# Performance work log

Hardware: AMD Instinct MI355X
Metric: run time of the kernel (lower is better)

Reference implementation:

```python
import jax, jax.numpy as jnp
import numpy as np

K = 64      # neighbor_num (subgraph size)
TOPK = 10   # topk for sparse adjacency scatter
DN = 10     # density_neighbor


def _build_graphs(indexes, features):
    # compute_knn: inner-product top-K neighbor table over all N samples
    N, D = features.shape
    sim = features @ features.T                      # [N, N]
    _, ori0 = jax.lax.top_k(sim, K)                  # [N, K] neighbor indices
    # density: all_sim[n] = sum_{i<DN} <f_n, f_{ori0[n,i]}> / (4*DN)
    g = features[ori0[:, :DN]]                       # [N, DN, D]
    all_sim = jnp.einsum('nd,nkd->n', features, g) / (4.0 * DN)
    exp_sim = jnp.exp(all_sim)                       # [N]

    rows = jnp.arange(K)[:, None]                    # [K,1]

    def build_one(idx):
        nbr = ori0[idx]                              # [K] neighbors of query idx
        feat = features[nbr]                         # [K, D]
        neigh = ori0[nbr][:, :TOPK]                  # [K, TOPK]
        A = (feat @ features.T) * exp_sim[None, :]   # [K, N] density-reweighted sims
        # scatter only the topk entries of each row into sparse tmp
        tmp = jnp.zeros((K, N), features.dtype).at[rows, neigh].set(A[rows, neigh])
        adj = tmp @ (tmp.T > 0).astype(features.dtype)   # [K, K]
        adj = jax.nn.softmax(adj, axis=1)
        x = feat - feat[0]                           # center on query node
        return x, adj

    return jax.vmap(build_one)(indexes)              # [B,K,D], [B,K,K]


def _gconv(x, adj, W, b):
    # GraphConv with MeanAggregator: out = relu(concat([x, adj@x]) @ W + b)
    agg = jnp.einsum('bij,bjd->bid', adj, x)
    cat = jnp.concatenate([x, agg], axis=-1)
    return jax.nn.relu(jnp.einsum('bkd,df->bkf', cat, W) + b)


def setup_inputs() -> dict:
    key = jax.random.key(0)
    ks = jax.random.split(key, 16)
    N, D, NHID = 8192, 2048, 1024
    feats = jax.random.normal(ks[0], (N, D), dtype=jnp.float32)
    feats = feats / jnp.linalg.norm(feats, axis=1, keepdims=True)  # L2-normalized embeddings
    p = lambda k, shape: jax.random.normal(k, shape, dtype=jnp.float32) * 0.02
    return {
        'indexes': jax.random.randint(ks[1], (64,), 0, N, dtype=jnp.int64) if jax.config.jax_enable_x64 else jax.random.randint(ks[1], (64,), 0, N, dtype=jnp.int32),
        'features': feats,
        'labels': jax.random.randint(ks[2], (N,), 0, 1000, dtype=jnp.int32),
        'domain': 1,
        'W1': p(ks[3], (2 * D, NHID)), 'b1': jnp.zeros((NHID,), jnp.float32),
        'W2': p(ks[4], (2 * NHID, 512)), 'b2': jnp.zeros((512,), jnp.float32),
        'W3': p(ks[5], (2 * 512, 256)), 'b3': jnp.zeros((256,), jnp.float32),
        'W4': p(ks[6], (2 * 256, 256)), 'b4': jnp.zeros((256,), jnp.float32),
        'Wc1': p(ks[7], (256, 256)), 'bc1': jnp.zeros((256,), jnp.float32),
        'prelu_a': jnp.full((256,), 0.25, jnp.float32),
        'Wc2': p(ks[8], (256, 2)), 'bc2': jnp.zeros((2,), jnp.float32),
    }


def reference(indexes, features, labels, domain, W1, b1, W2, b2, W3, b3, W4, b4,
              Wc1, bc1, prelu_a, Wc2, bc2):
    # labels only used for the (optional) loss branch; domain=1 path implemented.
    xs, adjs = _build_graphs(indexes, features)      # built under no_grad in torch
    h = _gconv(xs, adjs, W1, b1)
    h = _gconv(h, adjs, W2, b2)
    h = _gconv(h, adjs, W3, b3)
    h = _gconv(h, adjs, W4, b4)
    h = h @ Wc1 + bc1
    h = jnp.where(h > 0, h, prelu_a * h)             # PReLU(256)
    pred = h @ Wc2 + bc2                             # [B, K, 2]
    return pred
```

## Files before the change

### kernel.cpp

```cpp
#include <hip/hip_runtime.h>
#include <hip/hip_bf16.h>
#include <math.h>

#define NROWS 8192
#define DFEAT 2048
#define KSEL  64
#define CHK   2048

typedef unsigned long long u64;
typedef __attribute__((ext_vector_type(8))) short bf16x8;
typedef __attribute__((ext_vector_type(4))) float f32x4;

__device__ __forceinline__ u64 umax64(u64 a, u64 b) { return a > b ? a : b; }

__device__ __forceinline__ void split2(float v, ushort& h, ushort& l) {
  __hip_bfloat16 bh = __float2bfloat16(v);
  float r = v - __bfloat162float(bh);
  __hip_bfloat16 bl = __float2bfloat16(r);
  h = *(ushort*)&bh; l = *(ushort*)&bl;
}

__device__ __forceinline__ u64 mkkey_vi(float v, int i) {
  unsigned u = __float_as_uint(v);
  u = ((int)u < 0) ? ~u : (u | 0x80000000u);
  return ((u64)u << 32) | (u64)(0xFFFFFFFFu - (unsigned)i);
}

__global__ __launch_bounds__(256) void k_split(const float* __restrict__ F, ushort* __restrict__ H,
                                               ushort* __restrict__ M, ushort* __restrict__ L) {
  const size_t i0 = ((size_t)blockIdx.x * 256 + threadIdx.x) * 4;
  float4 x = *(const float4*)(F + i0);
  float xs[4] = {x.x, x.y, x.z, x.w};
  ushort h[4], m[4], l[4];
#pragma unroll
  for (int c = 0; c < 4; ++c) {
    float v = xs[c];
    __hip_bfloat16 bh = __float2bfloat16(v);
    float r1 = v - __bfloat162float(bh);
    __hip_bfloat16 bm = __float2bfloat16(r1);
    float r2 = r1 - __bfloat162float(bm);
    __hip_bfloat16 bl = __float2bfloat16(r2);
    h[c] = *(ushort*)&bh; m[c] = *(ushort*)&bm; l[c] = *(ushort*)&bl;
  }
  ushort4 vh = {h[0], h[1], h[2], h[3]};
  ushort4 vm = {m[0], m[1], m[2], m[3]};
  ushort4 vl = {l[0], l[1], l[2], l[3]};
  *(ushort4*)(H + i0) = vh;
  *(ushort4*)(M + i0) = vm;
  *(ushort4*)(L + i0) = vl;
}

__global__ __launch_bounds__(256) void k_simgemm_all(
    const ushort* __restrict__ FH, const ushort* __restrict__ FM, const ushort* __restrict__ FL,
    float* __restrict__ bufbase) {
  __shared__ ushort lds[6 * 4096];
  const int z = blockIdx.z;
  int ci = 0, rem = z;
  while (rem >= 4 - ci) { rem -= 4 - ci; ++ci; }
  const int cj = ci + rem;
  const int diag = (ci == cj);
  const int bj = blockIdx.x;
  const int bm = blockIdx.y;
  if (diag && bm > bj) return;
  const size_t TSZ = (size_t)CHK * CHK;
  float* TILE = bufbase + (size_t)(ci * 4 + cj) * TSZ;
  float* TILT = bufbase + (size_t)(cj * 4 + ci) * TSZ;
  const int t = threadIdx.x;
  const int w = t >> 6, l = t & 63;
  const int arow0 = ci * CHK + bm * 128;
  const int brow0 = cj * CHK + bj * 128;
  const int segr = l >> 2;
  const int segq_s = (l & 3) ^ ((l >> 3) & 3);
  const int fl15 = l & 15, fq = l >> 4;
  const int kswz = (fq ^ ((fl15 >> 1) & 3)) * 8;
  const int wr = w >> 1, wc = w & 1;
  const int mb = wr * 64, nb = wc * 64;

  f32x4 acc[4][4];
#pragma unroll
  for (int i = 0; i < 4; ++i)
#pragma unroll
    for (int j = 0; j < 4; ++j) acc[i][j] = (f32x4){0.f, 0.f, 0.f, 0.f};

  for (int k0 = 0; k0 < DFEAT; k0 += 32) {
    __syncthreads();
#pragma unroll
    for (int c = 0; c < 12; ++c) {
      const int cc = w * 12 + c;
      const int tt = cc >> 3;
      const int p = cc & 7;
      const int rowbase = (tt < 3) ? arow0 : brow0;
      const int sp = (tt < 3) ? tt : (tt - 3);
      const ushort* sel = (sp == 0) ? FH : ((sp == 1) ? FM : FL);
      const ushort* g = sel + (size_t)(rowbase + p * 16 + segr) * DFEAT + (k0 + segq_s * 8);
      __builtin_amdgcn_global_load_lds((const __attribute__((address_space(1))) unsigned int*)g,
                                       (__attribute__((address_space(3))) unsigned int*)&lds[tt * 4096 + p * 512],
                                       16, 0, 0);
    }
    __syncthreads();

    bf16x8 af[3][4];
    bf16x8 bg[3][4];
#pragma unroll
    for (int i = 0; i < 3; ++i)
#pragma unroll
      for (int fm = 0; fm < 4; ++fm)
        af[i][fm] = *(const bf16x8*)&lds[i * 4096 + (mb + fm * 16 + fl15) * 32 + kswz];
#pragma unroll
    for (int j = 0; j < 3; ++j)
#pragma unroll
      for (int fn = 0; fn < 4; ++fn)
        bg[j][fn] = *(const bf16x8*)&lds[(3 + j) * 4096 + (nb + fn * 16 + fl15) * 32 + kswz];

#pragma unroll
    for (int fm = 0; fm < 4; ++fm)
#pragma unroll
      for (int fn = 0; fn < 4; ++fn) {
        f32x4 a = acc[fm][fn];
        a = __builtin_amdgcn_mfma_f32_16x16x32_bf16(af[0][fm], bg[0][fn], a, 0, 0, 0);
        a = __builtin_amdgcn_mfma_f32_16x16x32_bf16(af[1][fm], bg[0][fn], a, 0, 0, 0);
        a = __builtin_amdgcn_mfma_f32_16x16x32_bf16(af[0][fm], bg[1][fn], a, 0, 0, 0);
        a = __builtin_amdgcn_mfma_f32_16x16x32_bf16(af[2][fm], bg[0][fn], a, 0, 0, 0);
        a = __builtin_amdgcn_mfma_f32_16x16x32_bf16(af[0][fm], bg[2][fn], a, 0, 0, 0);
        a = __builtin_amdgcn_mfma_f32_16x16x32_bf16(af[1][fm], bg[1][fn], a, 0, 0, 0);
        acc[fm][fn] = a;
      }
  }

  const bool doT = !(diag && bm == bj);
#pragma unroll
  for (int fm = 0; fm < 4; ++fm) {
    const int lm = bm * 128 + mb + fm * 16 + fq * 4;
#pragma unroll
    for (int fn = 0; fn < 4; ++fn) {
      const int col = bj * 128 + nb + fn * 16 + fl15;
#pragma unroll
      for (int r = 0; r < 4; ++r)
        TILE[(size_t)(lm + r) * CHK + col] = acc[fm][fn][r];
      if (doT) {
        float4 v = make_float4(acc[fm][fn][0], acc[fm][fn][1], acc[fm][fn][2], acc[fm][fn][3]);
        *(float4*)(TILT + (size_t)col * CHK + lm) = v;
      }
    }
  }
}

__global__ __launch_bounds__(256) void k_simgemm_pair(
    const ushort* __restrict__ FH, const ushort* __restrict__ FM, const ushort* __restrict__ FL,
    float* __restrict__ T0, float* __restrict__ T0T, int i0, int j0, int d0,
    float* __restrict__ T1, float* __restrict__ T1T, int i1, int j1, int d1) {
  __shared__ ushort lds[6 * 4096];
  const int z = blockIdx.z;
  float* TILE = z ? T1 : T0;
  float* TILT = z ? T1T : T0T;
  const int ci = z ? i1 : i0;
  const int cj = z ? j1 : j0;
  const int diag = z ? d1 : d0;
  const int bj = blockIdx.x;
  const int bm = blockIdx.y;
  if (diag && bm > bj) return;
  const int t = threadIdx.x;
  const int w = t >> 6, l = t & 63;
  const int arow0 = ci * CHK + bm * 128;
  const int brow0 = cj * CHK + bj * 128;
  const int segr = l >> 2;
  const int segq_s = (l & 3) ^ ((l >> 3) & 3);
  const int fl15 = l & 15, fq = l >> 4;
  const int kswz = (fq ^ ((fl15 >> 1) & 3)) * 8;
  const int wr = w >> 1, wc = w & 1;
  const int mb = wr * 64, nb = wc * 64;

  f32x4 acc[4][4];
#pragma unroll
  for (int i = 0; i < 4; ++i)
#pragma unroll
    for (int j = 0; j < 4; ++j) acc[i][j] = (f32x4){0.f, 0.f, 0.f, 0.f};

  for (int k0 = 0; k0 < DFEAT; k0 += 32) {
    __syncthreads();
#pragma unroll
    for (int c = 0; c < 12; ++c) {
      const int cc = w * 12 + c;
      const int tt = cc >> 3;
      const int p = cc & 7;
      const int rowbase = (tt < 3) ? arow0 : brow0;
      const int sp = (tt < 3) ? tt : (tt - 3);
      const ushort* sel = (sp == 0) ? FH : ((sp == 1) ? FM : FL);
      const ushort* g = sel + (size_t)(rowbase + p * 16 + segr) * DFEAT + (k0 + segq_s * 8);
      __builtin_amdgcn_global_load_lds((const __attribute__((address_space(1))) unsigned int*)g,
                                       (__attribute__((address_space(3))) unsigned int*)&lds[tt * 4096 + p * 512],
                                       16, 0, 0);
    }
    __syncthreads();

    bf16x8 af[3][4];
    bf16x8 bg[3][4];
#pragma unroll
    for (int i = 0; i < 3; ++i)
#pragma unroll
      for (int fm = 0; fm < 4; ++fm)
        af[i][fm] = *(const bf16x8*)&lds[i * 4096 + (mb + fm * 16 + fl15) * 32 + kswz];
#pragma unroll
    for (int j = 0; j < 3; ++j)
#pragma unroll
      for (int fn = 0; fn < 4; ++fn)
        bg[j][fn] = *(const bf16x8*)&lds[(3 + j) * 4096 + (nb + fn * 16 + fl15) * 32 + kswz];

#pragma unroll
    for (int fm = 0; fm < 4; ++fm)
#pragma unroll
      for (int fn = 0; fn < 4; ++fn) {
        f32x4 a = acc[fm][fn];
        a = __builtin_amdgcn_mfma_f32_16x16x32_bf16(af[0][fm], bg[0][fn], a, 0, 0, 0);
        a = __builtin_amdgcn_mfma_f32_16x16x32_bf16(af[1][fm], bg[0][fn], a, 0, 0, 0);
        a = __builtin_amdgcn_mfma_f32_16x16x32_bf16(af[0][fm], bg[1][fn], a, 0, 0, 0);
        a = __builtin_amdgcn_mfma_f32_16x16x32_bf16(af[2][fm], bg[0][fn], a, 0, 0, 0);
        a = __builtin_amdgcn_mfma_f32_16x16x32_bf16(af[0][fm], bg[2][fn], a, 0, 0, 0);
        a = __builtin_amdgcn_mfma_f32_16x16x32_bf16(af[1][fm], bg[1][fn], a, 0, 0, 0);
        acc[fm][fn] = a;
      }
  }

  const bool doT = (TILT != nullptr) && !(diag && bm == bj);
#pragma unroll
  for (int fm = 0; fm < 4; ++fm) {
    const int lm = bm * 128 + mb + fm * 16 + fq * 4;
#pragma unroll
    for (int fn = 0; fn < 4; ++fn) {
      const int col = bj * 128 + nb + fn * 16 + fl15;
#pragma unroll
      for (int r = 0; r < 4; ++r)
        TILE[(size_t)(lm + r) * CHK + col] = acc[fm][fn][r];
      if (doT) {
        float4 v = make_float4(acc[fm][fn][0], acc[fm][fn][1], acc[fm][fn][2], acc[fm][fn][3]);
        *(float4*)(TILT + (size_t)col * CHK + lm) = v;
      }
    }
  }
}

__global__ __launch_bounds__(256) void k_simgemm_mfma(
    const ushort* __restrict__ FH, const ushort* __restrict__ FM, const ushort* __restrict__ FL,
    float* __restrict__ C, int row0) {
  __shared__ ushort lds[6 * 4096];
  const int bj = blockIdx.x;
  const int bm = blockIdx.y;
  const int t = threadIdx.x;
  const int w = t >> 6, l = t & 63;
  const int arow0 = row0 + bm * 128;
  const int brow0 = bj * 128;
  const int segr = l >> 2;
  const int segq = l & 3;
  const int fl15 = l & 15, fq = l >> 4;
  const int wr = w >> 1, wc = w & 1;
  const int mb = wr * 64, nb = wc * 64;

  f32x4 acc[4][4];
#pragma unroll
  for (int i = 0; i < 4; ++i)
#pragma unroll
    for (int j = 0; j < 4; ++j) acc[i][j] = (f32x4){0.f, 0.f, 0.f, 0.f};

  for (int k0 = 0; k0 < DFEAT; k0 += 32) {
    __syncthreads();
#pragma unroll
    for (int c = 0; c < 12; ++c) {
      const int cc = w * 12 + c;
      const int tt = cc >> 3;
      const int p = cc & 7;
      const int rowbase = (tt < 3) ? arow0 : brow0;
      const int sp = (tt < 3) ? tt : (tt - 3);
      const ushort* sel = (sp == 0) ? FH : ((sp == 1) ? FM : FL);
      const ushort* g = sel + (size_t)(rowbase + p * 16 + segr) * DFEAT + (k0 + segq * 8);
      __builtin_amdgcn_global_load_lds((const __attribute__((address_space(1))) unsigned int*)g,
                                       (__attribute__((address_space(3))) unsigned int*)&lds[tt * 4096 + p * 512],
                                       16, 0, 0);
    }
    __syncthreads();

    bf16x8 af[3][4];
    bf16x8 bg[3][4];
    const int kcol = fq * 8;
#pragma unroll
    for (int i = 0; i < 3; ++i)
#pragma unroll
      for (int fm = 0; fm < 4; ++fm)
        af[i][fm] = *(const bf16x8*)&lds[i * 4096 + (mb + fm * 16 + fl15) * 32 + kcol];
#pragma unroll
    for (int j = 0; j < 3; ++j)
#pragma unroll
      for (int fn = 0; fn < 4; ++fn)
        bg[j][fn] = *(const bf16x8*)&lds[(3 + j) * 4096 + (nb + fn * 16 + fl15) * 32 + kcol];

#pragma unroll
    for (int fm = 0; fm < 4; ++fm)
#pragma unroll
      for (int fn = 0; fn < 4; ++fn) {
        f32x4 a = acc[fm][fn];
        a = __builtin_amdgcn_mfma_f32_16x16x32_bf16(af[0][fm], bg[0][fn], a, 0, 0, 0);
        a = __builtin_amdgcn_mfma_f32_16x16x32_bf16(af[1][fm], bg[0][fn], a, 0, 0, 0);
        a = __builtin_amdgcn_mfma_f32_16x16x32_bf16(af[0][fm], bg[1][fn], a, 0, 0, 0);
        a = __builtin_amdgcn_mfma_f32_16x16x32_bf16(af[2][fm], bg[0][fn], a, 0, 0, 0);
        a = __builtin_amdgcn_mfma_f32_16x16x32_bf16(af[0][fm], bg[2][fn], a, 0, 0, 0);
        a = __builtin_amdgcn_mfma_f32_16x16x32_bf16(af[1][fm], bg[1][fn], a, 0, 0, 0);
        acc[fm][fn] = a;
      }
  }

#pragma unroll
  for (int fm = 0; fm < 4; ++fm) {
    const int lm = bm * 128 + mb + fm * 16 + fq * 4;
#pragma unroll
    for (int fn = 0; fn < 4; ++fn) {
      const int col = bj * 128 + nb + fn * 16 + fl15;
#pragma unroll
      for (int r = 0; r < 4; ++r)
        C[(size_t)(lm + r) * NROWS + col] = acc[fm][fn][r];
    }
  }
}

__global__ __launch_bounds__(256) void k_gemm3(const ushort* __restrict__ AH, const ushort* __restrict__ AL,
                                               const ushort* __restrict__ BH, const ushort* __restrict__ BL,
                                               float* __restrict__ C, int K, int N) {
  __shared__ ushort lds[4 * 4096];
  const int bj = blockIdx.x, bm = blockIdx.y;
  const int t = threadIdx.x;
  const int w = t >> 6, l = t & 63;
  const int segr = l >> 2;
  const int segq_s = (l & 3) ^ ((l >> 3) & 3);
  const int fl15 = l & 15, fq = l >> 4;
  const int kswz = (fq ^ ((fl15 >> 1) & 3)) * 8;
  const int wr = w >> 1, wc = w & 1;
  const int mb = wr * 64, nb = wc * 64;

  f32x4 acc[4][4];
#pragma unroll
  for (int i = 0; i < 4; ++i)
#pragma unroll
    for (int j = 0; j < 4; ++j) acc[i][j] = (f32x4){0.f, 0.f, 0.f, 0.f};

  for (int k0 = 0; k0 < K; k0 += 32) {
    __syncthreads();
#pragma unroll
    for (int c = 0; c < 8; ++c) {
      const int s = w * 8 + c;
      const int tt = s >> 3;
      const int p = s & 7;
      const int rowbase = (tt < 2) ? (bm * 128) : (bj * 128);
      const ushort* sel = (tt == 0) ? AH : ((tt == 1) ? AL : ((tt == 2) ? BH : BL));
      const ushort* g = sel + (size_t)(rowbase + p * 16 + segr) * K + (k0 + segq_s * 8);
      __builtin_amdgcn_global_load_lds((const __attribute__((address_space(1))) unsigned int*)g,
                                       (__attribute__((address_space(3))) unsigned int*)&lds[s * 512],
                                       16, 0, 0);
    }
    __syncthreads();

    bf16x8 af[2][4];
    bf16x8 bg[2][4];
#pragma unroll
    for (int i = 0; i < 2; ++i)
#pragma unroll
      for (int fm = 0; fm < 4; ++fm)
        af[i][fm] = *(const bf16x8*)&lds[i * 4096 + (mb + fm * 16 + fl15) * 32 + kswz];
#pragma unroll
    for (int j = 0; j < 2; ++j)
#pragma unroll
      for (int fn = 0; fn < 4; ++fn)
        bg[j][fn] = *(const bf16x8*)&lds[(2 + j) * 4096 + (nb + fn * 16 + fl15) * 32 + kswz];

#pragma unroll
    for (int fm = 0; fm < 4; ++fm)
#pragma unroll
      for (int fn = 0; fn < 4; ++fn) {
        f32x4 a = acc[fm][fn];
        a = __builtin_amdgcn_mfma_f32_16x16x32_bf16(af[0][fm], bg[0][fn], a, 0, 0, 0);
        a = __builtin_amdgcn_mfma_f32_16x16x32_bf16(af[0][fm], bg[1][fn], a, 0, 0, 0);
        a = __builtin_amdgcn_mfma_f32_16x16x32_bf16(af[1][fm], bg[0][fn], a, 0, 0, 0);
        acc[fm][fn] = a;
      }
  }

#pragma unroll
  for (int fm = 0; fm < 4; ++fm) {
    const int row = bm * 128 + mb + fm * 16 + fq * 4;
#pragma unroll
    for (int fn = 0; fn < 4; ++fn) {
      const int col = bj * 128 + nb + fn * 16 + fl15;
#pragma unroll
      for (int r = 0; r < 4; ++r)
        C[(size_t)(row + r) * N + col] = acc[fm][fn][r];
    }
  }
}

__global__ __launch_bounds__(256) void k_init_topk(float* __restrict__ topv, int* __restrict__ topi) {
  const int i = blockIdx.x * 256 + threadIdx.x;
  topv[i] = -INFINITY;
  topi[i] = 0;
}

__device__ __forceinline__ void topk_merge_body(const float* src, int row, int colbase,
                                                float* topv, int* topi,
                                                unsigned* cnt, unsigned* nselp, u64* selbuf) {
  const int t = threadIdx.x;
  if (t < 64) cnt[t] = 0;
  if (t == 0) *nselp = 0;

  u64 k[9];
  int nk = 8;
#pragma unroll
  for (int q = 0; q < 8; ++q) {
    float v = src[t + 256 * q];
    k[q] = mkkey_vi(v, colbase + t + 256 * q);
  }
  k[8] = 0;
  if (t < 64) {
    k[8] = mkkey_vi(topv[(size_t)row * KSEL + t], topi[(size_t)row * KSEL + t]);
    nk = 9;
  }
  __syncthreads();

  u64 T64 = 0;
  for (int bit = 63; bit >= 0; --bit) {
    const u64 cand = T64 | (1ull << bit);
    unsigned c = 0;
#pragma unroll
    for (int q = 0; q < 9; ++q) c += (q < nk && k[q] >= cand) ? 1u : 0u;
#pragma unroll
    for (int s = 32; s > 0; s >>= 1) c += __shfl_down(c, s);
    if ((t & 63) == 0) atomicAdd(&cnt[bit], c);
    __syncthreads();
    const unsigned cb = cnt[bit];
    if (cb >= 64) T64 = cand;
    if (cb == 64) break;
  }

#pragma unroll
  for (int q = 0; q < 9; ++q) {
    if (q < nk && k[q] >= T64) {
      unsigned p = atomicAdd(nselp, 1u);
      if (p < 64) selbuf[p] = k[q];
    }
  }
  __syncthreads();

  if (t < 64) {
    u64 key = selbuf[t];
#pragma unroll
    for (int kk = 2; kk <= 64; kk <<= 1) {
#pragma unroll
      for (int j = kk >> 1; j > 0; j >>= 1) {
        u64 other = __shfl_xor(key, j);
        const bool dirDesc = ((t & kk) == 0);
        const bool upper = ((t & j) != 0);
        u64 mx = umax64(key, other);
        u64 mn = (key < other) ? key : other;
        key = (dirDesc ^ upper) ? mx : mn;
      }
    }
    const unsigned ui = (unsigned)(key >> 32);
    const float v = __uint_as_float((ui & 0x80000000u) ? (ui ^ 0x80000000u) : ~ui);
    const int idx = (int)(0xFFFFFFFFu - (unsigned)(key & 0xFFFFFFFFull));
    topv[(size_t)row * KSEL + t] = v;
    topi[(size_t)row * KSEL + t] = idx;
  }
}

__global__ __launch_bounds__(256) void k_topk_update4(const float* __restrict__ bufbase, int g,
                                                      float* __restrict__ topv, int* __restrict__ topi) {
  __shared__ unsigned cnt[64];
  __shared__ unsigned nsel;
  __shared__ u64 selbuf[64];
  const int r = blockIdx.y;
  const int c = (r + g) & 3;
  const size_t TSZ = (size_t)CHK * CHK;
  const float* src = bufbase + (size_t)(r * 4 + c) * TSZ + (size_t)blockIdx.x * CHK;
  topk_merge_body(src, r * CHK + blockIdx.x, c * CHK, topv, topi, cnt, &nsel, selbuf);
}

__global__ __launch_bounds__(256) void k_topk_update(const float* __restrict__ T, int rowbase, int colbase,
                                                     float* __restrict__ topv, int* __restrict__ topi) {
  __shared__ unsigned cnt[64];
  __shared__ unsigned nsel;
  __shared__ u64 selbuf[64];
  const float* src = T + (size_t)blockIdx.x * CHK;
  topk_merge_body(src, rowbase + blockIdx.x, colbase, topv, topi, cnt, &nsel, selbuf);
}

__global__ __launch_bounds__(256) void k_exps(const float* __restrict__ topv, float* __restrict__ exps) {
  const int r = blockIdx.x * 256 + threadIdx.x;
  float s = 0.f;
#pragma unroll
  for (int q = 0; q < 10; ++q) s += topv[(size_t)r * KSEL + q];
  exps[r] = expf(s / 40.0f);
}

__global__ __launch_bounds__(256) void k_topk(const float* __restrict__ simc,
                                              float* __restrict__ topv, int* __restrict__ topi,
                                              float* __restrict__ exps, int row0) {
  __shared__ float vals[NROWS];
  __shared__ u64 wmax[4];
  __shared__ float outv[KSEL];
  __shared__ int outi[KSEL];
  const int row = row0 + blockIdx.x;
  const int t = threadIdx.x;
  const float* src = simc + (size_t)blockIdx.x * NROWS;
  for (int i = t; i < NROWS; i += 256) vals[i] = src[i];
  __syncthreads();

  u64 lk = 0;
#pragma unroll
  for (int m = 0; m < 32; ++m) {
    int i = t + 256 * m;
    lk = umax64(lk, mkkey_vi(vals[i], i));
  }

  const int lane = t & 63, wv = t >> 6;
  for (int it = 0; it < KSEL; ++it) {
    u64 wk = lk;
#pragma unroll
    for (int s = 32; s > 0; s >>= 1) {
      u64 o = __shfl_xor(wk, s);
      wk = umax64(wk, o);
    }
    if (lane == 0) wmax[wv] = wk;
    __syncthreads();
    u64 g = umax64(umax64(wmax[0], wmax[1]), umax64(wmax[2], wmax[3]));
    const unsigned ui = (unsigned)(g >> 32);
    const float v = __uint_as_float((ui & 0x80000000u) ? (ui ^ 0x80000000u) : ~ui);
    const int idx = (int)(0xFFFFFFFFu - (unsigned)(g & 0xFFFFFFFFull));
    if (t == 0) { outv[it] = v; outi[it] = idx; }
    if (t == (idx & 255)) {
      vals[idx] = -INFINITY;
      u64 nl = 0;
#pragma unroll
      for (int m = 0; m < 32; ++m) {
        int i = t + 256 * m;
        nl = umax64(nl, mkkey_vi(vals[i], i));
      }
      lk = nl;
    }
    __syncthreads();
  }
  if (t < KSEL) {
    topv[(size_t)row * KSEL + t] = outv[t];
    topi[(size_t)row * KSEL + t] = outi[t];
  }
  if (t == 0) {
    float s = 0.f;
#pragma unroll
    for (int q = 0; q < 10; ++q) s += outv[q];
    exps[row] = expf(s / 40.0f);
  }
}

__global__ __launch_bounds__(256) void k_adj(const int* __restrict__ indexes,
                                             const float* __restrict__ topv, const int* __restrict__ topi,
                                             const float* __restrict__ exps, float* __restrict__ adj) {
  __shared__ int nbr[64];
  __shared__ int neigh[64][10];
  __shared__ float tv[64][10];
  __shared__ float adjL[64][64];
  const int b = blockIdx.x;
  const int t = threadIdx.x;
  const int idx = indexes[b];
  if (t < 64) nbr[t] = topi[(size_t)idx * KSEL + t];
  __syncthreads();
  for (int p = t; p < 640; p += 256) {
    const int r = p / 10, q = p - r * 10;
    const int m = nbr[r];
    const int c = topi[(size_t)m * KSEL + q];
    neigh[r][q] = c;
    tv[r][q] = topv[(size_t)m * KSEL + q] * exps[c];
  }
  __syncthreads();
  for (int p = t; p < 4096; p += 256) {
    const int i = p >> 6, j = p & 63;
    float s = 0.f;
#pragma unroll
    for (int q = 0; q < 10; ++q) {
      const int c = neigh[i][q];
      float add = 0.f;
      for (int s2 = 0; s2 < 10; ++s2) {
        if (neigh[j][s2] == c) { add = (tv[j][s2] > 0.f) ? tv[i][q] : 0.f; break; }
      }
      s += add;
    }
    adjL[i][j] = s;
  }
  __syncthreads();
  const int wv = t >> 6, lane = t & 63;
  for (int i = wv * 16; i < wv * 16 + 16; ++i) {
    float v = adjL[i][lane];
    float mx = v;
#pragma unroll
    for (int s = 32; s > 0; s >>= 1) mx = fmaxf(mx, __shfl_xor(mx, s));
    float e = expf(v - mx);
    float sum = e;
#pragma unroll
    for (int s = 32; s > 0; s >>= 1) sum += __shfl_xor(sum, s);
    adj[((size_t)b * 64 + i) * 64 + lane] = e / sum;
  }
}

__global__ __launch_bounds__(256) void k_xs_split(const int* __restrict__ indexes, const int* __restrict__ topi,
                                                  const float* __restrict__ F,
                                                  ushort* __restrict__ XH, ushort* __restrict__ XL) {
  const int b = blockIdx.y, r = blockIdx.x;
  const int t = threadIdx.x;
  const int idx = indexes[b];
  const int m  = topi[(size_t)idx * KSEL + r];
  const int m0 = topi[(size_t)idx * KSEL + 0];
  const float4* pa = (const float4*)(F + (size_t)m * DFEAT);
  const float4* pb = (const float4*)(F + (size_t)m0 * DFEAT);
  const size_t rowoff = ((size_t)b * 64 + r) * DFEAT;
#pragma unroll
  for (int it = 0; it < 2; ++it) {
    const int i = t + it * 256;
    float4 a = pa[i], c = pb[i];
    float d[4] = {a.x - c.x, a.y - c.y, a.z - c.z, a.w - c.w};
    ushort h[4], l[4];
#pragma unroll
    for (int q = 0; q < 4; ++q) split2(d[q], h[q], l[q]);
    ushort4 vh = {h[0], h[1], h[2], h[3]};
    ushort4 vl = {l[0], l[1], l[2], l[3]};
    *(ushort4*)(XH + rowoff + i * 4) = vh;
    *(ushort4*)(XL + rowoff + i * 4) = vl;
  }
}

__global__ __launch_bounds__(256) void k_wsplitT(const float* __restrict__ W,
                                                 ushort* __restrict__ WTH, ushort* __restrict__ WTL,
                                                 int K, int F) {
  __shared__ float tile[32][33];
  const int k0 = blockIdx.x * 32;
  const int n0 = blockIdx.y * 32;
  const int t = threadIdx.x;
  {
    const int r = t >> 3, cq = t & 7;
    const int srcRow = (n0 < F) ? (k0 + r) : (K + k0 + r);
    const int srcCol = (n0 < F) ? n0 : (n0 - F);
    float4 v = *(const float4*)(W + (size_t)srcRow * F + srcCol + cq * 4);
    tile[r][cq * 4 + 0] = v.x; tile[r][cq * 4 + 1] = v.y;
    tile[r][cq * 4 + 2] = v.z; tile[r][cq * 4 + 3] = v.w;
  }
  __syncthreads();
  {
    const int nl = t >> 3, kq = t & 7;
    ushort h[4], l[4];
#pragma unroll
    for (int i = 0; i < 4; ++i) split2(tile[kq * 4 + i][nl], h[i], l[i]);
    ushort4 vh = {h[0], h[1], h[2], h[3]};
    ushort4 vl = {l[0], l[1], l[2], l[3]};
    *(ushort4*)(WTH + (size_t)(n0 + nl) * K + k0 + kq * 4) = vh;
    *(ushort4*)(WTL + (size_t)(n0 + nl) * K + k0 + kq * 4) = vl;
  }
}

__global__ __launch_bounds__(256) void k_postlayer(const float* __restrict__ C, const float* __restrict__ adj,
                                                   const float* __restrict__ bias,
                                                   ushort* __restrict__ HH, ushort* __restrict__ HL, int F) {
  __shared__ float adjL[64 * 65];
  __shared__ float QL[64 * 66];
  const int f0 = blockIdx.x * 64;
  const int b = blockIdx.y;
  const int t = threadIdx.x;
  const int fc = t & 63, rg = t >> 6;
  const int twoF = 2 * F;
  for (int i = t; i < 4096; i += 256) {
    const int r = i >> 6, j = i & 63;
    adjL[r * 65 + j] = adj[(size_t)b * 4096 + i];
    QL[r * 66 + j] = C[(size_t)(b * 64 + r) * twoF + F + f0 + j];
  }
  __syncthreads();
  const float bv = bias[f0 + fc];
  for (int rr = 0; rr < 16; ++rr) {
    const int r = rg * 16 + rr;
    float s = 0.f;
#pragma unroll 8
    for (int j0 = 0; j0 < 64; ++j0) {
      const int j = (j0 + fc) & 63;
      s += adjL[r * 65 + j] * QL[j * 66 + fc];
    }
    const int row = b * 64 + r;
    float h = C[(size_t)row * twoF + f0 + fc] + s + bv;
    h = fmaxf(h, 0.f);
    ushort hh, hl;
    split2(h, hh, hl);
    HH[(size_t)row * F + f0 + fc] = hh;
    HL[(size_t)row * F + f0 + fc] = hl;
  }
}

__global__ __launch_bounds__(256) void k_final2(const float* __restrict__ C, const float* __restrict__ bc1,
                                                const float* __restrict__ pre, const float* __restrict__ Wc2,
                                                const float* __restrict__ bc2, float* __restrict__ outp) {
  __shared__ float w[512];
  __shared__ float red[512];
  const int t = threadIdx.x;
  for (int i = t; i < 512; i += 256) w[i] = Wc2[i];
  __syncthreads();
  const int m = blockIdx.x * 64 + (t >> 2);
  const int p = t & 3;
  const float* h = C + (size_t)m * 256;
  float s0 = 0.f, s1 = 0.f;
  for (int k = p * 64; k < p * 64 + 64; ++k) {
    float hv = h[k] + bc1[k];
    hv = (hv > 0.f) ? hv : pre[k] * hv;
    s0 += hv * w[k * 2];
    s1 += hv * w[k * 2 + 1];
  }
  red[t * 2] = s0; red[t * 2 + 1] = s1;
  __syncthreads();
  if (p == 0) {
    for (int q = 1; q < 4; ++q) { s0 += red[(t + q) * 2]; s1 += red[(t + q) * 2 + 1]; }
    outp[m * 2 + 0] = s0 + bc2[0];
    outp[m * 2 + 1] = s1 + bc2[1];
  }
}

extern "C" void kernel_launch(void* const* d_in, const int* in_sizes, int n_in,
                              void* d_out, int out_size, void* d_ws, size_t ws_size,
                              hipStream_t stream) {
  const int*   indexes = (const int*)d_in[0];
  const float* F   = (const float*)d_in[1];
  const float* W1  = (const float*)d_in[4];
  const float* b1  = (const float*)d_in[5];
  const float* W2  = (const float*)d_in[6];
  const float* b2  = (const float*)d_in[7];
  const float* W3  = (const float*)d_in[8];
  const float* b3  = (const float*)d_in[9];
  const float* W4  = (const float*)d_in[10];
  const float* b4  = (const float*)d_in[11];
  const float* Wc1 = (const float*)d_in[12];
  const float* bc1 = (const float*)d_in[13];
  const float* pre = (const float*)d_in[14];
  const float* Wc2 = (const float*)d_in[15];
  const float* bc2 = (const float*)d_in[16];
  float* out = (float*)d_out;

  size_t off = 0;
  auto take = [&](size_t bytes) -> char* {
    char* q = (char*)d_ws + off;
    off += (bytes + 255) & ~(size_t)255;
    return q;
  };
  float* TOPV = (float*)take((size_t)NROWS * KSEL * 4);
  int*   TOPI = (int*)  take((size_t)NROWS * KSEL * 4);
  float* EXPS = (float*)take((size_t)NROWS * 4);
  float* ADJ  = (float*)take((size_t)64 * 64 * 64 * 4);
  char*  big  = (char*)d_ws + off;
  const size_t big_bytes = (ws_size > off) ? (ws_size - off) : 0;

  const size_t Mi = 1024 * 1024;
  const size_t Ki = 1024;
  const size_t splitBytes = (size_t)NROWS * DFEAT * 2;

  if (big_bytes >= 352 * Mi) {
    ushort* FH = (ushort*)big;
    ushort* FM = (ushort*)(big + splitBytes);
    ushort* FL = (ushort*)(big + 2 * splitBytes);
    float* BUFS = (float*)(big + 96 * Mi);
    k_split<<<NROWS * DFEAT / 1024, 256, 0, stream>>>(F, FH, FM, FL);
    k_init_topk<<<NROWS * KSEL / 256, 256, 0, stream>>>(TOPV, TOPI);
    k_simgemm_all<<<dim3(16, 16, 10), 256, 0, stream>>>(FH, FM, FL, BUFS);
    for (int g = 0; g < 4; ++g)
      k_topk_update4<<<dim3(CHK, 4), 256, 0, stream>>>(BUFS, g, TOPV, TOPI);
    k_exps<<<NROWS / 256, 256, 0, stream>>>(TOPV, EXPS);
  } else if (big_bytes >= 160 * Mi) {
    ushort* FH = (ushort*)big;
    ushort* FM = (ushort*)(big + splitBytes);
    ushort* FL = (ushort*)(big + 2 * splitBytes);
    float* TILE0  = (float*)(big + 96 * Mi);
    float* TILE0T = (float*)(big + 112 * Mi);
    float* TILE1  = (float*)(big + 128 * Mi);
    float* TILE1T = (float*)(big + 144 * Mi);
    k_split<<<NROWS * DFEAT / 1024, 256, 0, stream>>>(F, FH, FM, FL);
    k_init_topk<<<NROWS * KSEL / 256, 256, 0, stream>>>(TOPV, TOPI);
    const int pairs[10][2] = {{0,0},{0,1},{0,2},{0,3},{1,1},{1,2},{1,3},{2,2},{2,3},{3,3}};
    for (int b = 0; b < 5; ++b) {
      const int ia = pairs[2*b][0],   ja = pairs[2*b][1];
      const int ib = pairs[2*b+1][0], jb = pairs[2*b+1][1];
      const int da = (ia == ja), db = (ib == jb);
      k_simgemm_pair<<<dim3(16, 16, 2), 256, 0, stream>>>(
          FH, FM, FL,
          TILE0, da ? TILE0 : TILE0T, ia, ja, da,
          TILE1, db ? TILE1 : TILE1T, ib, jb, db);
      k_topk_update<<<CHK, 256, 0, stream>>>(TILE0, ia * CHK, ja * CHK, TOPV, TOPI);
      if (!da) k_topk_update<<<CHK, 256, 0, stream>>>(TILE0T, ja * CHK, ia * CHK, TOPV, TOPI);
      k_topk_update<<<CHK, 256, 0, stream>>>(TILE1, ib * CHK, jb * CHK, TOPV, TOPI);
      if (!db) k_topk_update<<<CHK, 256, 0, stream>>>(TILE1T, jb * CHK, ib * CHK, TOPV, TOPI);
    }
    k_exps<<<NROWS / 256, 256, 0, stream>>>(TOPV, EXPS);
  } else {
    int fchunk = 0;
    for (int c = 2048; c >= 512; c >>= 1) {
      if (3 * splitBytes + (size_t)c * NROWS * 4 <= big_bytes) { fchunk = c; break; }
    }
    if (fchunk == 0) {
      hipMemsetAsync(d_out, 0, (size_t)out_size * 4, stream);
      return;
    }
    ushort* FH = (ushort*)big;
    ushort* FM = (ushort*)(big + splitBytes);
    ushort* FL = (ushort*)(big + 2 * splitBytes);
    float* SIMC = (float*)(big + 3 * splitBytes);
    k_split<<<NROWS * DFEAT / 1024, 256, 0, stream>>>(F, FH, FM, FL);
    for (int r0 = 0; r0 < NROWS; r0 += fchunk) {
      k_simgemm_mfma<<<dim3(64, fchunk / 128), 256, 0, stream>>>(FH, FM, FL, SIMC, r0);
      k_topk<<<fchunk, 256, 0, stream>>>(SIMC, TOPV, TOPI, EXPS, r0);
    }
  }
  k_adj<<<64, 256, 0, stream>>>(indexes, TOPV, TOPI, EXPS, ADJ);

  ushort* XH   = (ushort*)(big);
  ushort* XL   = (ushort*)(big + 16 * Mi);
  ushort* WT1H = (ushort*)(big + 32 * Mi);
  ushort* WT1L = (ushort*)(big + 40 * Mi);
  ushort* WT2H = (ushort*)(big + 48 * Mi);
  ushort* WT2L = (ushort*)(big + 50 * Mi);
  ushort* WT3H = (ushort*)(big + 52 * Mi);
  ushort* WT3L = (ushort*)(big + 52 * Mi + 512 * Ki);
  ushort* WT4H = (ushort*)(big + 53 * Mi);
  ushort* WT4L = (ushort*)(big + 53 * Mi + 256 * Ki);
  ushort* WTcH = (ushort*)(big + 53 * Mi + 512 * Ki);
  ushort* WTcL = (ushort*)(big + 53 * Mi + 640 * Ki);
  float*  CBUF = (float*)(big + 54 * Mi);
  ushort* H1H  = (ushort*)(big + 32 * Mi);
  ushort* H1L  = (ushort*)(big + 40 * Mi);
  ushort* H2H  = (ushort*)(big);
  ushort* H2L  = (ushort*)(big + 4 * Mi);
  ushort* H3H  = (ushort*)(big + 8 * Mi);
  ushort* H3L  = (ushort*)(big + 10 * Mi);
  ushort* H4H  = (ushort*)(big + 12 * Mi);
  ushort* H4L  = (ushort*)(big + 14 * Mi);

  k_wsplitT<<<dim3(2048 / 32, 2048 / 32), 256, 0, stream>>>(W1, WT1H, WT1L, 2048, 1024);
  k_wsplitT<<<dim3(1024 / 32, 1024 / 32), 256, 0, stream>>>(W2, WT2H, WT2L, 1024, 512);
  k_wsplitT<<<dim3(512 / 32, 512 / 32), 256, 0, stream>>>(W3, WT3H, WT3L, 512, 256);
  k_wsplitT<<<dim3(256 / 32, 512 / 32), 256, 0, stream>>>(W4, WT4H, WT4L, 256, 256);
  k_wsplitT<<<dim3(256 / 32, 256 / 32), 256, 0, stream>>>(Wc1, WTcH, WTcL, 256, 256);

  k_xs_split<<<dim3(64, 64), 256, 0, stream>>>(indexes, TOPI, F, XH, XL);

  k_gemm3<<<dim3(16, 32), 256, 0, stream>>>(XH, XL, WT1H, WT1L, CBUF, 2048, 2048);
  k_postlayer<<<dim3(16, 64), 256, 0, stream>>>(CBUF, ADJ, b1, H1H, H1L, 1024);
  k_gemm3<<<dim3(8, 32), 256, 0, stream>>>(H1H, H1L, WT2H, WT2L, CBUF, 1024, 1024);
  k_postlayer<<<dim3(8, 64), 256, 0, stream>>>(CBUF, ADJ, b2, H2H, H2L, 512);
  k_gemm3<<<dim3(4, 32), 256, 0, stream>>>(H2H, H2L, WT3H, WT3L, CBUF, 512, 512);
  k_postlayer<<<dim3(4, 64), 256, 0, stream>>>(CBUF, ADJ, b3, H3H, H3L, 256);
  k_gemm3<<<dim3(4, 32), 256, 0, stream>>>(H3H, H3L, WT4H, WT4L, CBUF, 256, 512);
  k_postlayer<<<dim3(4, 64), 256, 0, stream>>>(CBUF, ADJ, b4, H4H, H4L, 256);
  k_gemm3<<<dim3(2, 32), 256, 0, stream>>>(H4H, H4L, WTcH, WTcL, CBUF, 256, 256);
  k_final2<<<64, 256, 0, stream>>>(CBUF, bc1, pre, Wc2, bc2, out);
}
```

Before: 1.661 ms.

## Restructure similarity/top-k schedule into four rounds over four reused tile buffers

```diff
diff --git a/kernel.cpp b/kernel.cpp
--- a/kernel.cpp
+++ b/kernel.cpp
@@ -50,21 +50,107 @@
   *(ushort4*)(L + i0) = vl;
 }
 
-__global__ __launch_bounds__(256) void k_simgemm_all(
+__global__ __launch_bounds__(256) void k_simgemm_diag(
     const ushort* __restrict__ FH, const ushort* __restrict__ FM, const ushort* __restrict__ FL,
     float* __restrict__ bufbase) {
   __shared__ ushort lds[6 * 4096];
-  const int z = blockIdx.z;
-  int ci = 0, rem = z;
-  while (rem >= 4 - ci) { rem -= 4 - ci; ++ci; }
-  const int cj = ci + rem;
-  const int diag = (ci == cj);
+  const int cc = blockIdx.z;
   const int bj = blockIdx.x;
   const int bm = blockIdx.y;
-  if (diag && bm > bj) return;
-  const size_t TSZ = (size_t)CHK * CHK;
-  float* TILE = bufbase + (size_t)(ci * 4 + cj) * TSZ;
-  float* TILT = bufbase + (size_t)(cj * 4 + ci) * TSZ;
+  if (bm > bj) return;
+  float* TILE = bufbase + (size_t)cc * CHK * CHK;
+  const int t = threadIdx.x;
+  const int w = t >> 6, l = t & 63;
+  const int arow0 = cc * CHK + bm * 128;
+  const int brow0 = cc * CHK + bj * 128;
+  const int segr = l >> 2;
+  const int segq_s = (l & 3) ^ ((l >> 3) & 3);
+  const int fl15 = l & 15, fq = l >> 4;
+  const int kswz = (fq ^ ((fl15 >> 1) & 3)) * 8;
+  const int wr = w >> 1, wc = w & 1;
+  const int mb = wr * 64, nb = wc * 64;
+
+  f32x4 acc[4][4];
+#pragma unroll
+  for (int i = 0; i < 4; ++i)
+#pragma unroll
+    for (int j = 0; j < 4; ++j) acc[i][j] = (f32x4){0.f, 0.f, 0.f, 0.f};
+
+  for (int k0 = 0; k0 < DFEAT; k0 += 32) {
+    __syncthreads();
+#pragma unroll
+    for (int c = 0; c < 12; ++c) {
+      const int cidx = w * 12 + c;
+      const int tt = cidx >> 3;
+      const int p = cidx & 7;
+      const int rowbase = (tt < 3) ? arow0 : brow0;
+      const int sp = (tt < 3) ? tt : (tt - 3);
+      const ushort* sel = (sp == 0) ? FH : ((sp == 1) ? FM : FL);
+      const ushort* g = sel + (size_t)(rowbase + p * 16 + segr) * DFEAT + (k0 + segq_s * 8);
+      __builtin_amdgcn_global_load_lds((const __attribute__((address_space(1))) unsigned int*)g,
+                                       (__attribute__((address_space(3))) unsigned int*)&lds[tt * 4096 + p * 512],
+                                       16, 0, 0);
+    }
+    __syncthreads();
+
+    bf16x8 af[3][4];
+    bf16x8 bg[3][4];
+#pragma unroll
+    for (int i = 0; i < 3; ++i)
+#pragma unroll
+      for (int fm = 0; fm < 4; ++fm)
+        af[i][fm] = *(const bf16x8*)&lds[i * 4096 + (mb + fm * 16 + fl15) * 32 + kswz];
+#pragma unroll
+    for (int j = 0; j < 3; ++j)
+#pragma unroll
+      for (int fn = 0; fn < 4; ++fn)
+        bg[j][fn] = *(const bf16x8*)&lds[(3 + j) * 4096 + (nb + fn * 16 + fl15) * 32 + kswz];
+
+#pragma unroll
+    for (int fm = 0; fm < 4; ++fm)
+#pragma unroll
+      for (int fn = 0; fn < 4; ++fn) {
+        f32x4 a = acc[fm][fn];
+        a = __builtin_amdgcn_mfma_f32_16x16x32_bf16(af[0][fm], bg[0][fn], a, 0, 0, 0);
+        a = __builtin_amdgcn_mfma_f32_16x16x32_bf16(af[1][fm], bg[0][fn], a, 0, 0, 0);
+        a = __builtin_amdgcn_mfma_f32_16x16x32_bf16(af[0][fm], bg[1][fn], a, 0, 0, 0);
+        a = __builtin_amdgcn_mfma_f32_16x16x32_bf16(af[2][fm], bg[0][fn], a, 0, 0, 0);
+        a = __builtin_amdgcn_mfma_f32_16x16x32_bf16(af[0][fm], bg[2][fn], a, 0, 0, 0);
+        a = __builtin_amdgcn_mfma_f32_16x16x32_bf16(af[1][fm], bg[1][fn], a, 0, 0, 0);
+        acc[fm][fn] = a;
+      }
+  }
+
+  const bool doT = (bm != bj);
+#pragma unroll
+  for (int fm = 0; fm < 4; ++fm) {
+    const int lm = bm * 128 + mb + fm * 16 + fq * 4;
+#pragma unroll
+    for (int fn = 0; fn < 4; ++fn) {
+      const int col = bj * 128 + nb + fn * 16 + fl15;
+#pragma unroll
+      for (int r = 0; r < 4; ++r)
+        TILE[(size_t)(lm + r) * CHK + col] = acc[fm][fn][r];
+      if (doT) {
+        float4 v = make_float4(acc[fm][fn][0], acc[fm][fn][1], acc[fm][fn][2], acc[fm][fn][3]);
+        *(float4*)(TILE + (size_t)col * CHK + lm) = v;
+      }
+    }
+  }
+}
+
+__global__ __launch_bounds__(256) void k_simgemm_pair(
+    const ushort* __restrict__ FH, const ushort* __restrict__ FM, const ushort* __restrict__ FL,
+    float* __restrict__ T0, float* __restrict__ T0T, int i0, int j0,
+    float* __restrict__ T1, float* __restrict__ T1T, int i1, int j1) {
+  __shared__ ushort lds[6 * 4096];
+  const int z = blockIdx.z;
+  float* TILE = z ? T1 : T0;
+  float* TILT = z ? T1T : T0T;
+  const int ci = z ? i1 : i0;
+  const int cj = z ? j1 : j0;
+  const int bj = blockIdx.x;
+  const int bm = blockIdx.y;
   const int t = threadIdx.x;
   const int w = t >> 6, l = t & 63;
   const int arow0 = ci * CHK + bm * 128;
@@ -127,7 +213,6 @@
       }
   }
 
-  const bool doT = !(diag && bm == bj);
 #pragma unroll
   for (int fm = 0; fm < 4; ++fm) {
     const int lm = bm * 128 + mb + fm * 16 + fq * 4;
@@ -137,104 +222,8 @@
 #pragma unroll
       for (int r = 0; r < 4; ++r)
         TILE[(size_t)(lm + r) * CHK + col] = acc[fm][fn][r];
-      if (doT) {
-        float4 v = make_float4(acc[fm][fn][0], acc[fm][fn][1], acc[fm][fn][2], acc[fm][fn][3]);
-        *(float4*)(TILT + (size_t)col * CHK + lm) = v;
-      }
-    }
-  }
-}
-
-__global__ __launch_bounds__(256) void k_simgemm_pair(
-    const ushort* __restrict__ FH, const ushort* __restrict__ FM, const ushort* __restrict__ FL,
-    float* __restrict__ T0, float* __restrict__ T0T, int i0, int j0, int d0,
-    float* __restrict__ T1, float* __restrict__ T1T, int i1, int j1, int d1) {
-  __shared__ ushort lds[6 * 4096];
-  const int z = blockIdx.z;
-  float* TILE = z ? T1 : T0;
-  float* TILT = z ? T1T : T0T;
-  const int ci = z ? i1 : i0;
-  const int cj = z ? j1 : j0;
-  const int diag = z ? d1 : d0;
-  const int bj = blockIdx.x;
-  const int bm = blockIdx.y;
-  if (diag && bm > bj) return;
-  const int t = threadIdx.x;
-  const int w = t >> 6, l = t & 63;
-  const int arow0 = ci * CHK + bm * 128;
-  const int brow0 = cj * CHK + bj * 128;
-  const int segr = l >> 2;
-  const int segq_s = (l & 3) ^ ((l >> 3) & 3);
-  const int fl15 = l & 15, fq = l >> 4;
-  const int kswz = (fq ^ ((fl15 >> 1) & 3)) * 8;
-  const int wr = w >> 1, wc = w & 1;
-  const int mb = wr * 64, nb = wc * 64;
-
-  f32x4 acc[4][4];
-#pragma unroll
-  for (int i = 0; i < 4; ++i)
-#pragma unroll
-    for (int j = 0; j < 4; ++j) acc[i][j] = (f32x4){0.f, 0.f, 0.f, 0.f};
-
-  for (int k0 = 0; k0 < DFEAT; k0 += 32) {
-    __syncthreads();
-#pragma unroll
-    for (int c = 0; c < 12; ++c) {
-      const int cc = w * 12 + c;
-      const int tt = cc >> 3;
-      const int p = cc & 7;
-      const int rowbase = (tt < 3) ? arow0 : brow0;
-      const int sp = (tt < 3) ? tt : (tt - 3);
-      const ushort* sel = (sp == 0) ? FH : ((sp == 1) ? FM : FL);
-      const ushort* g = sel + (size_t)(rowbase + p * 16 + segr) * DFEAT + (k0 + segq_s * 8);
-      __builtin_amdgcn_global_load_lds((const __attribute__((address_space(1))) unsigned int*)g,
-                                       (__attribute__((address_space(3))) unsigned int*)&lds[tt * 4096 + p * 512],
-                                       16, 0, 0);
-    }
-    __syncthreads();
-
-    bf16x8 af[3][4];
-    bf16x8 bg[3][4];
-#pragma unroll
-    for (int i = 0; i < 3; ++i)
-#pragma unroll
-      for (int fm = 0; fm < 4; ++fm)
-        af[i][fm] = *(const bf16x8*)&lds[i * 4096 + (mb + fm * 16 + fl15) * 32 + kswz];
-#pragma unroll
-    for (int j = 0; j < 3; ++j)
-#pragma unroll
-      for (int fn = 0; fn < 4; ++fn)
-        bg[j][fn] = *(const bf16x8*)&lds[(3 + j) * 4096 + (nb + fn * 16 + fl15) * 32 + kswz];
-
-#pragma unroll
-    for (int fm = 0; fm < 4; ++fm)
-#pragma unroll
-      for (int fn = 0; fn < 4; ++fn) {
-        f32x4 a = acc[fm][fn];
-        a = __builtin_amdgcn_mfma_f32_16x16x32_bf16(af[0][fm], bg[0][fn], a, 0, 0, 0);
-        a = __builtin_amdgcn_mfma_f32_16x16x32_bf16(af[1][fm], bg[0][fn], a, 0, 0, 0);
-        a = __builtin_amdgcn_mfma_f32_16x16x32_bf16(af[0][fm], bg[1][fn], a, 0, 0, 0);
-        a = __builtin_amdgcn_mfma_f32_16x16x32_bf16(af[2][fm], bg[0][fn], a, 0, 0, 0);
-        a = __builtin_amdgcn_mfma_f32_16x16x32_bf16(af[0][fm], bg[2][fn], a, 0, 0, 0);
-        a = __builtin_amdgcn_mfma_f32_16x16x32_bf16(af[1][fm], bg[1][fn], a, 0, 0, 0);
-        acc[fm][fn] = a;
-      }
-  }
-
-  const bool doT = (TILT != nullptr) && !(diag && bm == bj);
-#pragma unroll
-  for (int fm = 0; fm < 4; ++fm) {
-    const int lm = bm * 128 + mb + fm * 16 + fq * 4;
-#pragma unroll
-    for (int fn = 0; fn < 4; ++fn) {
-      const int col = bj * 128 + nb + fn * 16 + fl15;
-#pragma unroll
-      for (int r = 0; r < 4; ++r)
-        TILE[(size_t)(lm + r) * CHK + col] = acc[fm][fn][r];
-      if (doT) {
-        float4 v = make_float4(acc[fm][fn][0], acc[fm][fn][1], acc[fm][fn][2], acc[fm][fn][3]);
-        *(float4*)(TILT + (size_t)col * CHK + lm) = v;
-      }
+      float4 v = make_float4(acc[fm][fn][0], acc[fm][fn][1], acc[fm][fn][2], acc[fm][fn][3]);
+      *(float4*)(TILT + (size_t)col * CHK + lm) = v;
     }
   }
 }
@@ -467,25 +456,19 @@
   }
 }
 
-__global__ __launch_bounds__(256) void k_topk_update4(const float* __restrict__ bufbase, int g,
-                                                      float* __restrict__ topv, int* __restrict__ topi) {
+__global__ __launch_bounds__(256) void k_topk_upd4(const float* __restrict__ bufbase,
+                                                   int b0, int b1, int b2, int b3,
+                                                   int c0, int c1, int c2, int c3,
+                                                   float* __restrict__ topv, int* __restrict__ topi) {
   __shared__ unsigned cnt[64];
   __shared__ unsigned nsel;
   __shared__ u64 selbuf[64];
-  const int r = blockIdx.y;
-  const int c = (r + g) & 3;
+  const int y = blockIdx.y;
+  const int bi = (y == 0) ? b0 : ((y == 1) ? b1 : ((y == 2) ? b2 : b3));
+  const int cc = (y == 0) ? c0 : ((y == 1) ? c1 : ((y == 2) ? c2 : c3));
   const size_t TSZ = (size_t)CHK * CHK;
-  const float* src = bufbase + (size_t)(r * 4 + c) * TSZ + (size_t)blockIdx.x * CHK;
-  topk_merge_body(src, r * CHK + blockIdx.x, c * CHK, topv, topi, cnt, &nsel, selbuf);
-}
-
-__global__ __launch_bounds__(256) void k_topk_update(const float* __restrict__ T, int rowbase, int colbase,
-                                                     float* __restrict__ topv, int* __restrict__ topi) {
-  __shared__ unsigned cnt[64];
-  __shared__ unsigned nsel;
-  __shared__ u64 selbuf[64];
-  const float* src = T + (size_t)blockIdx.x * CHK;
-  topk_merge_body(src, rowbase + blockIdx.x, colbase, topv, topi, cnt, &nsel, selbuf);
+  const float* src = bufbase + (size_t)bi * TSZ + (size_t)blockIdx.x * CHK;
+  topk_merge_body(src, y * CHK + blockIdx.x, cc * CHK, topv, topi, cnt, &nsel, selbuf);
 }
 
 __global__ __launch_bounds__(256) void k_exps(const float* __restrict__ topv, float* __restrict__ exps) {
@@ -756,42 +739,29 @@
   const size_t Mi = 1024 * 1024;
   const size_t Ki = 1024;
   const size_t splitBytes = (size_t)NROWS * DFEAT * 2;
-
-  if (big_bytes >= 352 * Mi) {
+  const size_t TSZ = (size_t)CHK * CHK;
+
+  if (big_bytes >= 160 * Mi) {
     ushort* FH = (ushort*)big;
     ushort* FM = (ushort*)(big + splitBytes);
     ushort* FL = (ushort*)(big + 2 * splitBytes);
     float* BUFS = (float*)(big + 96 * Mi);
     k_split<<<NROWS * DFEAT / 1024, 256, 0, stream>>>(F, FH, FM, FL);
     k_init_topk<<<NROWS * KSEL / 256, 256, 0, stream>>>(TOPV, TOPI);
-    k_simgemm_all<<<dim3(16, 16, 10), 256, 0, stream>>>(FH, FM, FL, BUFS);
-    for (int g = 0; g < 4; ++g)
-      k_topk_update4<<<dim3(CHK, 4), 256, 0, stream>>>(BUFS, g, TOPV, TOPI);
-    k_exps<<<NROWS / 256, 256, 0, stream>>>(TOPV, EXPS);
-  } else if (big_bytes >= 160 * Mi) {
-    ushort* FH = (ushort*)big;
-    ushort* FM = (ushort*)(big + splitBytes);
-    ushort* FL = (ushort*)(big + 2 * splitBytes);
-    float* TILE0  = (float*)(big + 96 * Mi);
-    float* TILE0T = (float*)(big + 112 * Mi);
-    float* TILE1  = (float*)(big + 128 * Mi);
-    float* TILE1T = (float*)(big + 144 * Mi);
-    k_split<<<NROWS * DFEAT / 1024, 256, 0, stream>>>(F, FH, FM, FL);
-    k_init_topk<<<NROWS * KSEL / 256, 256, 0, stream>>>(TOPV, TOPI);
-    const int pairs[10][2] = {{0,0},{0,1},{0,2},{0,3},{1,1},{1,2},{1,3},{2,2},{2,3},{3,3}};
-    for (int b = 0; b < 5; ++b) {
-      const int ia = pairs[2*b][0],   ja = pairs[2*b][1];
-      const int ib = pairs[2*b+1][0], jb = pairs[2*b+1][1];
-      const int da = (ia == ja), db = (ib == jb);
-      k_simgemm_pair<<<dim3(16, 16, 2), 256, 0, stream>>>(
-          FH, FM, FL,
-          TILE0, da ? TILE0 : TILE0T, ia, ja, da,
-          TILE1, db ? TILE1 : TILE1T, ib, jb, db);
-      k_topk_update<<<CHK, 256, 0, stream>>>(TILE0, ia * CHK, ja * CHK, TOPV, TOPI);
-      if (!da) k_topk_update<<<CHK, 256, 0, stream>>>(TILE0T, ja * CHK, ia * CHK, TOPV, TOPI);
-      k_topk_update<<<CHK, 256, 0, stream>>>(TILE1, ib * CHK, jb * CHK, TOPV, TOPI);
-      if (!db) k_topk_update<<<CHK, 256, 0, stream>>>(TILE1T, jb * CHK, ib * CHK, TOPV, TOPI);
-    }
+    k_simgemm_diag<<<dim3(16, 16, 4), 256, 0, stream>>>(FH, FM, FL, BUFS);
+    k_topk_upd4<<<dim3(CHK, 4), 256, 0, stream>>>(BUFS, 0, 1, 2, 3, 0, 1, 2, 3, TOPV, TOPI);
+    k_simgemm_pair<<<dim3(16, 16, 2), 256, 0, stream>>>(FH, FM, FL,
+        BUFS + 0 * TSZ, BUFS + 1 * TSZ, 0, 1,
+        BUFS + 2 * TSZ, BUFS + 3 * TSZ, 2, 3);
+    k_topk_upd4<<<dim3(CHK, 4), 256, 0, stream>>>(BUFS, 0, 1, 2, 3, 1, 0, 3, 2, TOPV, TOPI);
+    k_simgemm_pair<<<dim3(16, 16, 2), 256, 0, stream>>>(FH, FM, FL,
+        BUFS + 0 * TSZ, BUFS + 1 * TSZ, 0, 2,
+        BUFS + 2 * TSZ, BUFS + 3 * TSZ, 1, 3);
+    k_topk_upd4<<<dim3(CHK, 4), 256, 0, stream>>>(BUFS, 0, 2, 1, 3, 2, 3, 0, 1, TOPV, TOPI);
+    k_simgemm_pair<<<dim3(16, 16, 2), 256, 0, stream>>>(FH, FM, FL,
+        BUFS + 0 * TSZ, BUFS + 1 * TSZ, 0, 3,
+        BUFS + 2 * TSZ, BUFS + 3 * TSZ, 1, 2);
+    k_topk_upd4<<<dim3(CHK, 4), 256, 0, stream>>>(BUFS, 0, 2, 3, 1, 3, 2, 1, 0, TOPV, TOPI);
     k_exps<<<NROWS / 256, 256, 0, stream>>>(TOPV, EXPS);
   } else {
     int fchunk = 0;
```

Result: faster. 1.561 ms (-6.0%).
